# Performance work log

Hardware: AMD Instinct MI355X
Metric: run time of the kernel (lower is better)

The kernel has to match this reference:

```python
import jax, jax.numpy as jnp
import numpy as np

B, S, D, H = 2, 2048, 2048, 16
DK = D // H  # 128


def _rope(x, cos, sin):
    # x: [B,S,H,DK]; pairs (x0,x1),(x2,x3),... rotated as complex numbers
    xr = x[..., 0::2]  # [B,S,H,DK/2]
    xi = x[..., 1::2]
    yr = xr * cos - xi * sin
    yi = xr * sin + xi * cos
    y = jnp.stack([yr, yi], axis=-1)  # [B,S,H,DK/2,2]
    return y.reshape(x.shape)


def setup_inputs() -> dict:
    key = jax.random.key(0)
    ks = jax.random.split(key, 12)
    sc = 1.0 / np.sqrt(D)
    q = jax.random.normal(ks[0], (B, S, D), jnp.float32)
    k = jax.random.normal(ks[1], (B, S, D), jnp.float32)
    v = jax.random.normal(ks[2], (B, S, D), jnp.float32)
    mask = jnp.tril(jnp.ones((S, S), jnp.int32))[None, None]  # causal [1,1,S,S]
    # standard RoPE angles: pos * theta^(-2i/dk)
    theta = 10000.0 ** (-jnp.arange(0, DK, 2, dtype=jnp.float32) / DK)  # [DK/2]
    freqs_angles = jnp.arange(S, dtype=jnp.float32)[:, None] * theta[None, :]  # [S,DK/2]
    wq = jax.random.normal(ks[3], (D, D), jnp.float32) * sc
    bq = jax.random.normal(ks[4], (D,), jnp.float32) * 0.01
    wk = jax.random.normal(ks[5], (D, D), jnp.float32) * sc
    bk = jax.random.normal(ks[6], (D,), jnp.float32) * 0.01
    wv = jax.random.normal(ks[7], (D, D), jnp.float32) * sc
    bv = jax.random.normal(ks[8], (D,), jnp.float32) * 0.01
    wo = jax.random.normal(ks[9], (D, D), jnp.float32) * sc
    bo = jax.random.normal(ks[10], (D,), jnp.float32) * 0.01
    return dict(q=q, k=k, v=v, mask=mask, freqs_angles=freqs_angles,
                wq=wq, bq=bq, wk=wk, bk=bk, wv=wv, bv=bv, wo=wo, bo=bo)


def reference(q, k, v, mask, freqs_angles, wq, bq, wk, bk, wv, bv, wo, bo):
    query = q @ wq.T + bq
    key_ = k @ wk.T + bk
    value = v @ wv.T + bv
    query = query.reshape(B, S, H, DK)
    key_ = key_.reshape(B, S, H, DK)
    value = value.reshape(B, S, H, DK).transpose(0, 2, 1, 3)  # [B,H,S,DK]
    cos = jnp.cos(freqs_angles)[None, :, None, :]  # [1,S,1,DK/2]
    sin = jnp.sin(freqs_angles)[None, :, None, :]
    query = _rope(query, cos, sin).transpose(0, 2, 1, 3)  # [B,H,S,DK]
    key_ = _rope(key_, cos, sin).transpose(0, 2, 1, 3)
    scores = jnp.einsum('bhqd,bhkd->bhqk', query, key_) / jnp.sqrt(jnp.float32(DK))
    scores = jnp.where(mask == 0, jnp.float32(-1e9), scores)
    attn = jax.nn.softmax(scores, axis=-1)  # dropout p=0.0 -> identity
    x = jnp.einsum('bhqk,bhkd->bhqd', attn, value)
    x = x.transpose(0, 2, 1, 3).reshape(B, S, D)
    return x @ wo.T + bo
```

## Files before the change

kernel.cpp:

```cpp
#include <hip/hip_runtime.h>
#include <hip/hip_bf16.h>

#define BB 2
#define SS 2048
#define DD 2048
#define HH 16
#define DKK 128
#define MM (BB*SS)

typedef unsigned short u16;
typedef short bf16x8 __attribute__((ext_vector_type(8)));
typedef unsigned short u16x8 __attribute__((ext_vector_type(8)));
typedef float f32x4 __attribute__((ext_vector_type(4)));

static __device__ __forceinline__ f32x4 mfma_bf16(bf16x8 a, bf16x8 b, f32x4 c) {
  return __builtin_amdgcn_mfma_f32_16x16x32_bf16(a, b, c, 0, 0, 0);
}

static __device__ __forceinline__ u16 f2b(float f) {
  unsigned int u = __float_as_uint(f);
  u = (u + 0x7FFFu + ((u >> 16) & 1u)) >> 16;
  return (u16)u;
}

static __device__ __forceinline__ u16 f2bq(float f) {
  unsigned int r;
  asm("v_cvt_pk_bf16_f32 %0, %1, %2" : "=v"(r) : "v"(f), "v"(f));
  return (u16)r;
}

static __device__ __forceinline__ void gl16(const u16* g, u16* l) {
  __builtin_amdgcn_global_load_lds(
      (const __attribute__((address_space(1))) unsigned int*)(const void*)g,
      (__attribute__((address_space(3))) unsigned int*)(void*)l, 16, 0, 0);
}

struct F2BArgs { const float* src[7]; u16* dst[7]; const float* fa; float* cs; };
__global__ __launch_bounds__(256) void k_f2bf_all(F2BArgs a) {
  int bid = blockIdx.x;
  if (bid >= 20480) {
    const int t0 = ((bid - 20480) * 256 + threadIdx.x) * 8;
    float4 a0 = *reinterpret_cast<const float4*>(a.fa + t0);
    float4 a1 = *reinterpret_cast<const float4*>(a.fa + t0 + 4);
    float4 o0, o1, o2, o3;
    o0.x = cosf(a0.x); o0.y = sinf(a0.x); o0.z = cosf(a0.y); o0.w = sinf(a0.y);
    o1.x = cosf(a0.z); o1.y = sinf(a0.z); o1.z = cosf(a0.w); o1.w = sinf(a0.w);
    o2.x = cosf(a1.x); o2.y = sinf(a1.x); o2.z = cosf(a1.y); o2.w = sinf(a1.y);
    o3.x = cosf(a1.z); o3.y = sinf(a1.z); o3.z = cosf(a1.w); o3.w = sinf(a1.w);
    float* out = a.cs + 2 * t0;
    *reinterpret_cast<float4*>(out)      = o0;
    *reinterpret_cast<float4*>(out + 4)  = o1;
    *reinterpret_cast<float4*>(out + 8)  = o2;
    *reinterpret_cast<float4*>(out + 12) = o3;
    return;
  }
  int buf, local;
  if (bid < 12288) { buf = bid >> 12; local = bid & 4095; }
  else { int t = bid - 12288; buf = 3 + (t >> 11); local = t & 2047; }
  const int i = (local * 256 + threadIdx.x) * 8;
  const float* in = a.src[buf];
  float4 v0 = *reinterpret_cast<const float4*>(in + i);
  float4 v1 = *reinterpret_cast<const float4*>(in + i + 4);
  u16x8 o;
  o[0]=f2b(v0.x); o[1]=f2b(v0.y); o[2]=f2b(v0.z); o[3]=f2b(v0.w);
  o[4]=f2b(v1.x); o[5]=f2b(v1.y); o[6]=f2b(v1.z); o[7]=f2b(v1.w);
  *reinterpret_cast<u16x8*>(a.dst[buf] + i) = o;
}

struct GemmJob { const u16* A; const u16* W; const float* bias; void* out; int mode; };
struct GemmArgs { GemmJob job[3]; };

__global__ __launch_bounds__(256, 2) void k_gemm3(GemmArgs ga, const float* __restrict__ cs) {
  const GemmJob J = ga.job[blockIdx.z];
  const u16* __restrict__ A = J.A;
  const u16* __restrict__ W = J.W;
  const int mode = J.mode;
  const int K = DD, N = DD;
  const int KT = K / 64;

  __shared__ __align__(16) u16 sA[2][128 * 64];
  __shared__ __align__(16) u16 sB[2][128 * 64];
  const int tid = threadIdx.x;
  const int l  = tid & 63;
  const int w  = tid >> 6;
  const int wr = w >> 1, wc = w & 1;
  const int bm = blockIdx.x * 128, bn = blockIdx.y * 128;
  const int lr = l & 15;
  const int lg = l >> 4;

  f32x4 acc[4][4];
#pragma unroll
  for (int mi = 0; mi < 4; mi++)
#pragma unroll
    for (int ni = 0; ni < 4; ni++)
#pragma unroll
      for (int j = 0; j < 4; j++) acc[mi][ni][j] = 0.0f;

  const int srcx = ((l & 7) * 8) ^ ((l >> 3) * 8);
  const u16* gAl = A + (size_t)(bm + w*32 + (l >> 3)) * K + srcx;
  const u16* gBl = W + (size_t)(bn + w*32 + (l >> 3)) * K + srcx;

  const int rx = (lr & 7) * 8;

  auto stage = [&](int kt) {
    u16* dA = &sA[kt & 1][(w * 32) * 64];
    u16* dB = &sB[kt & 1][(w * 32) * 64];
    const int k0 = kt * 64;
#pragma unroll
    for (int i = 0; i < 4; i++) gl16(gAl + (size_t)i*8*K + k0, dA + i * 512);
#pragma unroll
    for (int i = 0; i < 4; i++) gl16(gBl + (size_t)i*8*K + k0, dB + i * 512);
  };

  stage(0);
  __syncthreads();

#pragma unroll 1
  for (int t = 0; t < KT; t++) {
    if (t + 1 < KT) stage(t + 1);
    const u16* a_ = sA[t & 1];
    const u16* b_ = sB[t & 1];
#pragma unroll
    for (int kk = 0; kk < 2; kk++) {
      bf16x8 af[4], bfv[4];
#pragma unroll
      for (int i = 0; i < 4; i++)
        af[i]  = *reinterpret_cast<const bf16x8*>(
            a_ + (wr*64 + i*16 + lr) * 64 + ((kk*32 + lg*8) ^ rx));
#pragma unroll
      for (int i = 0; i < 4; i++)
        bfv[i] = *reinterpret_cast<const bf16x8*>(
            b_ + (wc*64 + i*16 + lr) * 64 + ((kk*32 + lg*8) ^ rx));
#pragma unroll
      for (int mi = 0; mi < 4; mi++)
#pragma unroll
        for (int ni = 0; ni < 4; ni++)
          acc[mi][ni] = mfma_bf16(af[mi], bfv[ni], acc[mi][ni]);
    }
    __syncthreads();
  }

#pragma unroll
  for (int mi = 0; mi < 4; mi++) {
#pragma unroll
    for (int ni = 0; ni < 4; ni++) {
      const int col = bn + wc*64 + ni*16 + lr;
      const float bv = J.bias[col];
#pragma unroll
      for (int r = 0; r < 4; r++) {
        const int row = bm + wr*64 + mi*16 + lg*4 + r;
        float v = acc[mi][ni][r] + bv;
        if (mode & 1) {
          const int s  = row & (SS - 1);
          const int dk = col & (DKK - 1);
          const int p  = dk >> 1;
          const float2 csv = *reinterpret_cast<const float2*>(cs + (size_t)(s*64 + p)*2);
          const float other = __shfl_xor(v, 1);
          const float sgn = (dk & 1) ? csv.y : -csv.y;
          v = v * csv.x + other * sgn;
          if (mode == 3) v *= 0.12751744f;
        }
        if (mode == 2) {
          reinterpret_cast<float*>(J.out)[(size_t)row * N + col] = v;
        } else {
          reinterpret_cast<u16*>(J.out)[(size_t)row * N + col] = f2b(v);
        }
      }
    }
  }
}

__global__ __launch_bounds__(256, 2) void k_attn(const u16* __restrict__ Qp,
                                                 const u16* __restrict__ Kp,
                                                 const u16* __restrict__ Vp,
                                                 u16* __restrict__ Op) {
  const int bid = blockIdx.x;
  int bh, qt;
  if (bid < 256) { bh = bid & 31; qt = 15 - (bid >> 5); }
  else { int b2 = bid - 256; bh = b2 & 31; qt = b2 >> 5; }
  const int h  = bh & 15;
  const int b  = bh >> 4;
  const int tid = threadIdx.x;
  const int l  = tid & 63, w = tid >> 6;
  const int lr = l & 15, lg = l >> 4;

  __shared__ __align__(16) u16 Klds[2 * 64 * 128];
  __shared__ __align__(16) u16 VT[128 * 64];
  __shared__ __align__(16) u16 PL[4][32][72];

  int koff[4];
#pragma unroll
  for (int i = 0; i < 4; i++) {
    const int row = w*16 + i*4 + (l >> 4);
    koff[i] = row * DD + (((l & 15) * 8) ^ ((row & 7) * 8));
  }
  const u16* kbase = Kp + (size_t)b * SS * DD + h * DKK;

  const int k0v = (tid >> 5) * 8;
  const int d0  = (tid & 31) * 4;
  const u16* vbase = Vp + (size_t)b * SS * DD + h * DKK + (size_t)k0v * DD + d0;

  uint2 vr[8];

  auto stageK = [&](int nk, int bufq) {
    const u16* kb = kbase + (size_t)nk * (64 * DD);
    u16* dst = Klds + bufq * 8192 + (w * 16) * 128;
#pragma unroll
    for (int i = 0; i < 4; i++) gl16(kb + koff[i], dst + i * 512);
  };
  auto prefV = [&](int nk) {
    const u16* vb = vbase + (size_t)nk * (64 * DD);
#pragma unroll
    for (int c = 0; c < 8; c++) vr[c] = *reinterpret_cast<const uint2*>(vb + c * DD);
  };

  int cur = 0;
  stageK(0, 0);
  prefV(0);

  bf16x8 qf[2][4];
#pragma unroll
  for (int mt = 0; mt < 2; mt++) {
    const size_t qrow = (size_t)(b*SS + qt*128 + w*32 + mt*16 + lr) * DD + h*DKK;
#pragma unroll
    for (int kk = 0; kk < 4; kk++)
      qf[mt][kk] = *reinterpret_cast<const bf16x8*>(Qp + qrow + kk*32 + lg*8);
  }

  float m[2][4], lsum[2][4];
  f32x4 oacc[2][8];
#pragma unroll
  for (int mt = 0; mt < 2; mt++)
#pragma unroll
    for (int r = 0; r < 4; r++) { m[mt][r] = -INFINITY; lsum[mt][r] = 0.0f; }
#pragma unroll
  for (int mt = 0; mt < 2; mt++)
#pragma unroll
    for (int dt = 0; dt < 8; dt++)
#pragma unroll
      for (int jj = 0; jj < 4; jj++) oacc[mt][dt][jj] = 0.0f;

  const int kvmax = 2 * qt + 1;
#pragma unroll 1
  for (int kv = 0; kv <= kvmax; kv++) {
    __syncthreads();
#pragma unroll
    for (int dj = 0; dj < 4; dj++) {
      const int row = d0 + dj;
      const int col = k0v ^ (((row ^ (row >> 3)) & 7) * 8);
      u16x8 pk;
#pragma unroll
      for (int j = 0; j < 8; j++) pk[j] = reinterpret_cast<const u16*>(&vr[j])[dj];
      *reinterpret_cast<u16x8*>(VT + row * 64 + col) = pk;
    }
    __syncthreads();

    const bool hasnext = (kv < kvmax);
    if (hasnext) {
      prefV(kv + 1);
      stageK(kv + 1, cur ^ 1);
    }

    f32x4 sa[2][4];
#pragma unroll
    for (int mt = 0; mt < 2; mt++)
#pragma unroll
      for (int kt = 0; kt < 4; kt++)
#pragma unroll
        for (int jj = 0; jj < 4; jj++) sa[mt][kt][jj] = 0.0f;
    const u16* kl = Klds + cur * 8192;
    __builtin_amdgcn_s_setprio(1);
#pragma unroll
    for (int kk = 0; kk < 4; kk++) {
#pragma unroll
      for (int kt = 0; kt < 4; kt++) {
        const int row = kt*16 + lr;
        const bf16x8 kf = *reinterpret_cast<const bf16x8*>(
            kl + row * 128 + ((kk*32 + lg*8) ^ ((row & 7) * 8)));
#pragma unroll
        for (int mt = 0; mt < 2; mt++)
          sa[mt][kt] = mfma_bf16(qf[mt][kk], kf, sa[mt][kt]);
      }
    }
    __builtin_amdgcn_s_setprio(0);

    if (kv >= 2 * qt) {
#pragma unroll
      for (int kt = 0; kt < 4; kt++) {
        const int key = kv*64 + kt*16 + lr;
#pragma unroll
        for (int mt = 0; mt < 2; mt++)
#pragma unroll
          for (int r = 0; r < 4; r++) {
            const int qv = qt*128 + w*32 + mt*16 + lg*4 + r;
            if (key > qv) sa[mt][kt][r] = -1e9f;
          }
      }
    }

    float pm[2][4];
#pragma unroll
    for (int mt = 0; mt < 2; mt++)
#pragma unroll
      for (int r = 0; r < 4; r++)
        pm[mt][r] = fmaxf(fmaxf(sa[mt][0][r], sa[mt][1][r]),
                          fmaxf(sa[mt][2][r], sa[mt][3][r]));
    bool ok = true;
#pragma unroll
    for (int mt = 0; mt < 2; mt++)
#pragma unroll
      for (int r = 0; r < 4; r++) ok = ok && (pm[mt][r] <= m[mt][r] + 8.0f);
    if (!__all(ok)) {
#pragma unroll
      for (int mt = 0; mt < 2; mt++)
#pragma unroll
        for (int r = 0; r < 4; r++) {
          float t = pm[mt][r];
#pragma unroll
          for (int d = 1; d < 16; d <<= 1) t = fmaxf(t, __shfl_xor(t, d));
          const float mnew = fmaxf(m[mt][r], t);
          const float corr = exp2f(m[mt][r] - mnew);
          lsum[mt][r] *= corr;
#pragma unroll
          for (int dt = 0; dt < 8; dt++) oacc[mt][dt][r] *= corr;
          m[mt][r] = mnew;
        }
    }

#pragma unroll
    for (int mt = 0; mt < 2; mt++)
#pragma unroll
      for (int r = 0; r < 4; r++) {
        float rs = 0.0f;
#pragma unroll
        for (int kt = 0; kt < 4; kt++) {
          const float e = exp2f(sa[mt][kt][r] - m[mt][r]);
          rs += e;
          PL[w][mt*16 + lg*4 + r][kt*16 + lr] = f2bq(e);
        }
        lsum[mt][r] += rs;
      }

    __builtin_amdgcn_s_setprio(1);
#pragma unroll
    for (int kk2 = 0; kk2 < 2; kk2++) {
      bf16x8 pa[2];
#pragma unroll
      for (int mt = 0; mt < 2; mt++)
        pa[mt] = *reinterpret_cast<const bf16x8*>(&PL[w][mt*16 + lr][kk2*32 + lg*8]);
#pragma unroll
      for (int dt = 0; dt < 8; dt++) {
        const int row = dt*16 + lr;
        const bf16x8 vb = *reinterpret_cast<const bf16x8*>(
            VT + row * 64 + ((kk2*32 + lg*8) ^ (((row ^ (row >> 3)) & 7) * 8)));
#pragma unroll
        for (int mt = 0; mt < 2; mt++)
          oacc[mt][dt] = mfma_bf16(pa[mt], vb, oacc[mt][dt]);
      }
    }
    __builtin_amdgcn_s_setprio(0);

    if (hasnext) cur ^= 1;
  }

  float inv[2][4];
#pragma unroll
  for (int mt = 0; mt < 2; mt++)
#pragma unroll
    for (int r = 0; r < 4; r++) {
      float t = lsum[mt][r];
#pragma unroll
      for (int d = 1; d < 16; d <<= 1) t += __shfl_xor(t, d);
      inv[mt][r] = 1.0f / t;
    }
#pragma unroll
  for (int mt = 0; mt < 2; mt++)
#pragma unroll
    for (int dt = 0; dt < 8; dt++)
#pragma unroll
      for (int r = 0; r < 4; r++) {
        const size_t row = (size_t)(b*SS + qt*128 + w*32 + mt*16 + lg*4 + r);
        Op[row * DD + h*DKK + dt*16 + lr] = f2bq(oacc[mt][dt][r] * inv[mt][r]);
      }
}

extern "C" void kernel_launch(void* const* d_in, const int* in_sizes, int n_in,
                              void* d_out, int out_size, void* d_ws, size_t ws_size,
                              hipStream_t stream) {
  const float* q  = (const float*)d_in[0];
  const float* k  = (const float*)d_in[1];
  const float* v  = (const float*)d_in[2];
  const float* fa = (const float*)d_in[4];
  const float* wq = (const float*)d_in[5];
  const float* bq = (const float*)d_in[6];
  const float* wk = (const float*)d_in[7];
  const float* bk = (const float*)d_in[8];
  const float* wv = (const float*)d_in[9];
  const float* bv = (const float*)d_in[10];
  const float* wo = (const float*)d_in[11];
  const float* bo = (const float*)d_in[12];

  float* cs = (float*)d_ws;
  u16* bf = (u16*)((char*)d_ws + (size_t)262144 * sizeof(float));
  const size_t NX = (size_t)MM * DD;
  const size_t NW = (size_t)DD * DD;
  u16* q_bf  = bf;
  u16* k_bf  = q_bf + NX;
  u16* v_bf  = k_bf + NX;
  u16* wq_bf = v_bf + NX;
  u16* wk_bf = wq_bf + NW;
  u16* wv_bf = wk_bf + NW;
  u16* wo_bf = wv_bf + NW;
  u16* Qp    = wo_bf + NW;
  u16* Kp    = Qp + NX;
  u16* Vp    = Kp + NX;
  u16* Ao    = Vp + NX;

  F2BArgs fa7;
  fa7.src[0] = q;  fa7.dst[0] = q_bf;
  fa7.src[1] = k;  fa7.dst[1] = k_bf;
  fa7.src[2] = v;  fa7.dst[2] = v_bf;
  fa7.src[3] = wq; fa7.dst[3] = wq_bf;
  fa7.src[4] = wk; fa7.dst[4] = wk_bf;
  fa7.src[5] = wv; fa7.dst[5] = wv_bf;
  fa7.src[6] = wo; fa7.dst[6] = wo_bf;
  fa7.fa = fa;     fa7.cs = cs;
  k_f2bf_all<<<dim3(20544), 256, 0, stream>>>(fa7);

  GemmArgs gq;
  gq.job[0] = GemmJob{ q_bf, wq_bf, bq, (void*)Qp, 3 };
  gq.job[1] = GemmJob{ k_bf, wk_bf, bk, (void*)Kp, 1 };
  gq.job[2] = GemmJob{ v_bf, wv_bf, bv, (void*)Vp, 0 };
  k_gemm3<<<dim3(MM/128, DD/128, 3), 256, 0, stream>>>(gq, cs);

  k_attn<<<dim3(512), 256, 0, stream>>>(Qp, Kp, Vp, Ao);

  GemmArgs go;
  go.job[0] = GemmJob{ Ao, wo_bf, bo, d_out, 2 };
  go.job[1] = go.job[0];
  go.job[2] = go.job[0];
  k_gemm3<<<dim3(MM/128, DD/128, 1), 256, 0, stream>>>(go, cs);
}
```

Baseline: 310.8 us.

## Fuse fp32-to-bf16 activation conversion into QKV GEMM A-tile loading

The QKV projection GEMM now reads fp32 q/k/v directly, converting to bf16 in registers with packed cvt and writing swizzled tiles into LDS after the MFMA loop. The prep kernel converts only weights and computes cos/sin, avoiding a full write-and-reread of the bf16 activation copies. The cost is doubled A-operand global traffic per tile, with repeated reads across N tiles, plus extra register use and loss of direct-to-LDS loads for A.

New measurement: 375.9 us. 21.0% more time.

```diff
diff --git a/kernel.cpp b/kernel.cpp
--- a/kernel.cpp
+++ b/kernel.cpp
@@ -23,11 +23,12 @@
   return (u16)u;
 }
 
-static __device__ __forceinline__ u16 f2bq(float f) {
+static __device__ __forceinline__ unsigned int cvt2(float lo, float hi) {
   unsigned int r;
-  asm("v_cvt_pk_bf16_f32 %0, %1, %2" : "=v"(r) : "v"(f), "v"(f));
-  return (u16)r;
-}
+  asm("v_cvt_pk_bf16_f32 %0, %1, %2" : "=v"(r) : "v"(lo), "v"(hi));
+  return r;
+}
+static __device__ __forceinline__ u16 f2bq(float f) { return (u16)cvt2(f, f); }
 
 static __device__ __forceinline__ void gl16(const u16* g, u16* l) {
   __builtin_amdgcn_global_load_lds(
@@ -35,11 +36,11 @@
       (__attribute__((address_space(3))) unsigned int*)(void*)l, 16, 0, 0);
 }
 
-struct F2BArgs { const float* src[7]; u16* dst[7]; const float* fa; float* cs; };
-__global__ __launch_bounds__(256) void k_f2bf_all(F2BArgs a) {
+struct F2BArgs { const float* src[4]; u16* dst[4]; const float* fa; float* cs; };
+__global__ __launch_bounds__(256) void k_f2bf_w(F2BArgs a) {
   int bid = blockIdx.x;
-  if (bid >= 20480) {
-    const int t0 = ((bid - 20480) * 256 + threadIdx.x) * 8;
+  if (bid >= 8192) {
+    const int t0 = ((bid - 8192) * 256 + threadIdx.x) * 8;
     float4 a0 = *reinterpret_cast<const float4*>(a.fa + t0);
     float4 a1 = *reinterpret_cast<const float4*>(a.fa + t0 + 4);
     float4 o0, o1, o2, o3;
@@ -54,9 +55,8 @@
     *reinterpret_cast<float4*>(out + 12) = o3;
     return;
   }
-  int buf, local;
-  if (bid < 12288) { buf = bid >> 12; local = bid & 4095; }
-  else { int t = bid - 12288; buf = 3 + (t >> 11); local = t & 2047; }
+  const int buf = bid >> 11;
+  const int local = bid & 2047;
   const int i = (local * 256 + threadIdx.x) * 8;
   const float* in = a.src[buf];
   float4 v0 = *reinterpret_cast<const float4*>(in + i);
@@ -67,12 +67,12 @@
   *reinterpret_cast<u16x8*>(a.dst[buf] + i) = o;
 }
 
-struct GemmJob { const u16* A; const u16* W; const float* bias; void* out; int mode; };
+struct GemmJob { const void* A; const u16* W; const float* bias; void* out; int mode; };
 struct GemmArgs { GemmJob job[3]; };
 
-__global__ __launch_bounds__(256, 2) void k_gemm3(GemmArgs ga, const float* __restrict__ cs) {
+template <int AF32>
+__global__ __launch_bounds__(256, 2) void k_gemmT(GemmArgs ga, const float* __restrict__ cs) {
   const GemmJob J = ga.job[blockIdx.z];
-  const u16* __restrict__ A = J.A;
   const u16* __restrict__ W = J.W;
   const int mode = J.mode;
   const int K = DD, N = DD;
@@ -97,27 +97,61 @@
       for (int j = 0; j < 4; j++) acc[mi][ni][j] = 0.0f;
 
   const int srcx = ((l & 7) * 8) ^ ((l >> 3) * 8);
-  const u16* gAl = A + (size_t)(bm + w*32 + (l >> 3)) * K + srcx;
+  const int cx   = srcx;
+  const u16* gAl16 = (const u16*)J.A + (size_t)(bm + w*32 + (l >> 3)) * K + srcx;
+  const float* gA32 = (const float*)J.A + (size_t)(bm + w*32 + (l >> 3)) * K + (l & 7) * 8;
   const u16* gBl = W + (size_t)(bn + w*32 + (l >> 3)) * K + srcx;
+  const int rowbase = (w*32 + (l >> 3)) * 64;
 
   const int rx = (lr & 7) * 8;
 
-  auto stage = [&](int kt) {
+  float4 ar[4][2];
+
+  auto loadA32 = [&](int kt) {
+    const float* g = gA32 + kt * 64;
+#pragma unroll
+    for (int i = 0; i < 4; i++) {
+      ar[i][0] = *reinterpret_cast<const float4*>(g + (size_t)i*8*K);
+      ar[i][1] = *reinterpret_cast<const float4*>(g + (size_t)i*8*K + 4);
+    }
+  };
+  auto writeA32 = [&](int kt) {
+    u16* dA = &sA[kt & 1][0];
+#pragma unroll
+    for (int i = 0; i < 4; i++) {
+      uint4 o;
+      o.x = cvt2(ar[i][0].x, ar[i][0].y);
+      o.y = cvt2(ar[i][0].z, ar[i][0].w);
+      o.z = cvt2(ar[i][1].x, ar[i][1].y);
+      o.w = cvt2(ar[i][1].z, ar[i][1].w);
+      *reinterpret_cast<uint4*>(dA + rowbase + i*8*64 + cx) = o;
+    }
+  };
+  auto stageA16 = [&](int kt) {
     u16* dA = &sA[kt & 1][(w * 32) * 64];
+    const int k0 = kt * 64;
+#pragma unroll
+    for (int i = 0; i < 4; i++) gl16(gAl16 + (size_t)i*8*K + k0, dA + i * 512);
+  };
+  auto stageB = [&](int kt) {
     u16* dB = &sB[kt & 1][(w * 32) * 64];
     const int k0 = kt * 64;
 #pragma unroll
-    for (int i = 0; i < 4; i++) gl16(gAl + (size_t)i*8*K + k0, dA + i * 512);
-#pragma unroll
     for (int i = 0; i < 4; i++) gl16(gBl + (size_t)i*8*K + k0, dB + i * 512);
   };
 
-  stage(0);
+  stageB(0);
+  if (AF32) { loadA32(0); writeA32(0); }
+  else      { stageA16(0); }
   __syncthreads();
 
 #pragma unroll 1
   for (int t = 0; t < KT; t++) {
-    if (t + 1 < KT) stage(t + 1);
+    if (t + 1 < KT) {
+      stageB(t + 1);
+      if (AF32) loadA32(t + 1);
+      else      stageA16(t + 1);
+    }
     const u16* a_ = sA[t & 1];
     const u16* b_ = sB[t & 1];
 #pragma unroll
@@ -137,6 +171,7 @@
         for (int ni = 0; ni < 4; ni++)
           acc[mi][ni] = mfma_bf16(af[mi], bfv[ni], acc[mi][ni]);
     }
+    if (AF32 && t + 1 < KT) writeA32(t + 1);
     __syncthreads();
   }
 
@@ -416,28 +451,25 @@
   u16* Vp    = Kp + NX;
   u16* Ao    = Vp + NX;
 
-  F2BArgs fa7;
-  fa7.src[0] = q;  fa7.dst[0] = q_bf;
-  fa7.src[1] = k;  fa7.dst[1] = k_bf;
-  fa7.src[2] = v;  fa7.dst[2] = v_bf;
-  fa7.src[3] = wq; fa7.dst[3] = wq_bf;
-  fa7.src[4] = wk; fa7.dst[4] = wk_bf;
-  fa7.src[5] = wv; fa7.dst[5] = wv_bf;
-  fa7.src[6] = wo; fa7.dst[6] = wo_bf;
-  fa7.fa = fa;     fa7.cs = cs;
-  k_f2bf_all<<<dim3(20544), 256, 0, stream>>>(fa7);
+  F2BArgs fw;
+  fw.src[0] = wq; fw.dst[0] = wq_bf;
+  fw.src[1] = wk; fw.dst[1] = wk_bf;
+  fw.src[2] = wv; fw.dst[2] = wv_bf;
+  fw.src[3] = wo; fw.dst[3] = wo_bf;
+  fw.fa = fa;     fw.cs = cs;
+  k_f2bf_w<<<dim3(8256), 256, 0, stream>>>(fw);
 
   GemmArgs gq;
-  gq.job[0] = GemmJob{ q_bf, wq_bf, bq, (void*)Qp, 3 };
-  gq.job[1] = GemmJob{ k_bf, wk_bf, bk, (void*)Kp, 1 };
-  gq.job[2] = GemmJob{ v_bf, wv_bf, bv, (void*)Vp, 0 };
-  k_gemm3<<<dim3(MM/128, DD/128, 3), 256, 0, stream>>>(gq, cs);
+  gq.job[0] = GemmJob{ (const void*)q, wq_bf, bq, (void*)Qp, 3 };
+  gq.job[1] = GemmJob{ (const void*)k, wk_bf, bk, (void*)Kp, 1 };
+  gq.job[2] = GemmJob{ (const void*)v, wv_bf, bv, (void*)Vp, 0 };
+  k_gemmT<1><<<dim3(MM/128, DD/128, 3), 256, 0, stream>>>(gq, cs);
 
   k_attn<<<dim3(512), 256, 0, stream>>>(Qp, Kp, Vp, Ao);
 
   GemmArgs go;
-  go.job[0] = GemmJob{ Ao, wo_bf, bo, d_out, 2 };
+  go.job[0] = GemmJob{ (const void*)Ao, wo_bf, bo, d_out, 2 };
   go.job[1] = go.job[0];
   go.job[2] = go.job[0];
-  k_gemm3<<<dim3(MM/128, DD/128, 1), 256, 0, stream>>>(go, cs);
-}
+  k_gemmT<0><<<dim3(MM/128, DD/128, 1), 256, 0, stream>>>(go, cs);
+}
```

## Halve attention query tile to 64 rows and double grid size

Applied to the files above, without the earlier changes.

The attention kernel now processes 64 query rows per block (16 per wave) instead of 128, launching 1024 blocks in longest-first order. This cuts per-block registers and causal waste on the diagonal tile, and gives more blocks to balance across CUs. In exchange, each K/V tile loaded into LDS is reused by half as many queries, so K/V global traffic and staging overhead per FLOP roughly double.

Result: faster. 304.3 us (-2.1%).

```diff
diff --git a/kernel.cpp b/kernel.cpp
--- a/kernel.cpp
+++ b/kernel.cpp
@@ -175,18 +175,18 @@
                                                  const u16* __restrict__ Vp,
                                                  u16* __restrict__ Op) {
   const int bid = blockIdx.x;
-  int bh, qt;
-  if (bid < 256) { bh = bid & 31; qt = 15 - (bid >> 5); }
-  else { int b2 = bid - 256; bh = b2 & 31; qt = b2 >> 5; }
+  const int j  = 31 - (bid >> 5);
+  const int bh = bid & 31;
   const int h  = bh & 15;
   const int b  = bh >> 4;
   const int tid = threadIdx.x;
   const int l  = tid & 63, w = tid >> 6;
   const int lr = l & 15, lg = l >> 4;
+  const int q0 = j * 64;
 
   __shared__ __align__(16) u16 Klds[2 * 64 * 128];
   __shared__ __align__(16) u16 VT[128 * 64];
-  __shared__ __align__(16) u16 PL[4][32][72];
+  __shared__ __align__(16) u16 PL[4][16][72];
 
   int koff[4];
 #pragma unroll
@@ -218,31 +218,25 @@
   stageK(0, 0);
   prefV(0);
 
-  bf16x8 qf[2][4];
-#pragma unroll
-  for (int mt = 0; mt < 2; mt++) {
-    const size_t qrow = (size_t)(b*SS + qt*128 + w*32 + mt*16 + lr) * DD + h*DKK;
+  bf16x8 qf[4];
+  {
+    const size_t qrow = (size_t)(b*SS + q0 + w*16 + lr) * DD + h*DKK;
 #pragma unroll
     for (int kk = 0; kk < 4; kk++)
-      qf[mt][kk] = *reinterpret_cast<const bf16x8*>(Qp + qrow + kk*32 + lg*8);
-  }
-
-  float m[2][4], lsum[2][4];
-  f32x4 oacc[2][8];
-#pragma unroll
-  for (int mt = 0; mt < 2; mt++)
-#pragma unroll
-    for (int r = 0; r < 4; r++) { m[mt][r] = -INFINITY; lsum[mt][r] = 0.0f; }
-#pragma unroll
-  for (int mt = 0; mt < 2; mt++)
-#pragma unroll
-    for (int dt = 0; dt < 8; dt++)
-#pragma unroll
-      for (int jj = 0; jj < 4; jj++) oacc[mt][dt][jj] = 0.0f;
-
-  const int kvmax = 2 * qt + 1;
+      qf[kk] = *reinterpret_cast<const bf16x8*>(Qp + qrow + kk*32 + lg*8);
+  }
+
+  float m[4], lsum[4];
+  f32x4 oacc[8];
+#pragma unroll
+  for (int r = 0; r < 4; r++) { m[r] = -INFINITY; lsum[r] = 0.0f; }
+#pragma unroll
+  for (int dt = 0; dt < 8; dt++)
+#pragma unroll
+    for (int jj = 0; jj < 4; jj++) oacc[dt][jj] = 0.0f;
+
 #pragma unroll 1
-  for (int kv = 0; kv <= kvmax; kv++) {
+  for (int kv = 0; kv <= j; kv++) {
     __syncthreads();
 #pragma unroll
     for (int dj = 0; dj < 4; dj++) {
@@ -250,24 +244,22 @@
       const int col = k0v ^ (((row ^ (row >> 3)) & 7) * 8);
       u16x8 pk;
 #pragma unroll
-      for (int j = 0; j < 8; j++) pk[j] = reinterpret_cast<const u16*>(&vr[j])[dj];
+      for (int jq = 0; jq < 8; jq++) pk[jq] = reinterpret_cast<const u16*>(&vr[jq])[dj];
       *reinterpret_cast<u16x8*>(VT + row * 64 + col) = pk;
     }
     __syncthreads();
 
-    const bool hasnext = (kv < kvmax);
+    const bool hasnext = (kv < j);
     if (hasnext) {
       prefV(kv + 1);
       stageK(kv + 1, cur ^ 1);
     }
 
-    f32x4 sa[2][4];
-#pragma unroll
-    for (int mt = 0; mt < 2; mt++)
-#pragma unroll
-      for (int kt = 0; kt < 4; kt++)
-#pragma unroll
-        for (int jj = 0; jj < 4; jj++) sa[mt][kt][jj] = 0.0f;
+    f32x4 sa[4];
+#pragma unroll
+    for (int kt = 0; kt < 4; kt++)
+#pragma unroll
+      for (int jj = 0; jj < 4; jj++) sa[kt][jj] = 0.0f;
     const u16* kl = Klds + cur * 8192;
     __builtin_amdgcn_s_setprio(1);
 #pragma unroll
@@ -277,85 +269,67 @@
         const int row = kt*16 + lr;
         const bf16x8 kf = *reinterpret_cast<const bf16x8*>(
             kl + row * 128 + ((kk*32 + lg*8) ^ ((row & 7) * 8)));
-#pragma unroll
-        for (int mt = 0; mt < 2; mt++)
-          sa[mt][kt] = mfma_bf16(qf[mt][kk], kf, sa[mt][kt]);
+        sa[kt] = mfma_bf16(qf[kk], kf, sa[kt]);
       }
     }
     __builtin_amdgcn_s_setprio(0);
 
-    if (kv >= 2 * qt) {
+    if (kv == j) {
 #pragma unroll
       for (int kt = 0; kt < 4; kt++) {
-        const int key = kv*64 + kt*16 + lr;
-#pragma unroll
-        for (int mt = 0; mt < 2; mt++)
-#pragma unroll
-          for (int r = 0; r < 4; r++) {
-            const int qv = qt*128 + w*32 + mt*16 + lg*4 + r;
-            if (key > qv) sa[mt][kt][r] = -1e9f;
-          }
-      }
-    }
-
-    float pm[2][4];
-#pragma unroll
-    for (int mt = 0; mt < 2; mt++)
-#pragma unroll
-      for (int r = 0; r < 4; r++)
-        pm[mt][r] = fmaxf(fmaxf(sa[mt][0][r], sa[mt][1][r]),
-                          fmaxf(sa[mt][2][r], sa[mt][3][r]));
+        const int key = kt*16 + lr;
+#pragma unroll
+        for (int r = 0; r < 4; r++) {
+          const int qv = w*16 + lg*4 + r;
+          if (key > qv) sa[kt][r] = -1e9f;
+        }
+      }
+    }
+
+    float pm[4];
+#pragma unroll
+    for (int r = 0; r < 4; r++)
+      pm[r] = fmaxf(fmaxf(sa[0][r], sa[1][r]), fmaxf(sa[2][r], sa[3][r]));
     bool ok = true;
 #pragma unroll
-    for (int mt = 0; mt < 2; mt++)
-#pragma unroll
-      for (int r = 0; r < 4; r++) ok = ok && (pm[mt][r] <= m[mt][r] + 8.0f);
+    for (int r = 0; r < 4; r++) ok = ok && (pm[r] <= m[r] + 8.0f);
     if (!__all(ok)) {
 #pragma unroll
-      for (int mt = 0; mt < 2; mt++)
-#pragma unroll
-        for (int r = 0; r < 4; r++) {
-          float t = pm[mt][r];
-#pragma unroll
-          for (int d = 1; d < 16; d <<= 1) t = fmaxf(t, __shfl_xor(t, d));
-          const float mnew = fmaxf(m[mt][r], t);
-          const float corr = exp2f(m[mt][r] - mnew);
-          lsum[mt][r] *= corr;
-#pragma unroll
-          for (int dt = 0; dt < 8; dt++) oacc[mt][dt][r] *= corr;
-          m[mt][r] = mnew;
-        }
-    }
-
-#pragma unroll
-    for (int mt = 0; mt < 2; mt++)
-#pragma unroll
       for (int r = 0; r < 4; r++) {
-        float rs = 0.0f;
-#pragma unroll
-        for (int kt = 0; kt < 4; kt++) {
-          const float e = exp2f(sa[mt][kt][r] - m[mt][r]);
-          rs += e;
-          PL[w][mt*16 + lg*4 + r][kt*16 + lr] = f2bq(e);
-        }
-        lsum[mt][r] += rs;
-      }
+        float t = pm[r];
+#pragma unroll
+        for (int d = 1; d < 16; d <<= 1) t = fmaxf(t, __shfl_xor(t, d));
+        const float mnew = fmaxf(m[r], t);
+        const float corr = exp2f(m[r] - mnew);
+        lsum[r] *= corr;
+#pragma unroll
+        for (int dt = 0; dt < 8; dt++) oacc[dt][r] *= corr;
+        m[r] = mnew;
+      }
+    }
+
+#pragma unroll
+    for (int r = 0; r < 4; r++) {
+      float rs = 0.0f;
+#pragma unroll
+      for (int kt = 0; kt < 4; kt++) {
+        const float e = exp2f(sa[kt][r] - m[r]);
+        rs += e;
+        PL[w][lg*4 + r][kt*16 + lr] = f2bq(e);
+      }
+      lsum[r] += rs;
+    }
 
     __builtin_amdgcn_s_setprio(1);
 #pragma unroll
     for (int kk2 = 0; kk2 < 2; kk2++) {
-      bf16x8 pa[2];
-#pragma unroll
-      for (int mt = 0; mt < 2; mt++)
-        pa[mt] = *reinterpret_cast<const bf16x8*>(&PL[w][mt*16 + lr][kk2*32 + lg*8]);
+      const bf16x8 pa = *reinterpret_cast<const bf16x8*>(&PL[w][lr][kk2*32 + lg*8]);
 #pragma unroll
       for (int dt = 0; dt < 8; dt++) {
         const int row = dt*16 + lr;
         const bf16x8 vb = *reinterpret_cast<const bf16x8*>(
             VT + row * 64 + ((kk2*32 + lg*8) ^ (((row ^ (row >> 3)) & 7) * 8)));
-#pragma unroll
-        for (int mt = 0; mt < 2; mt++)
-          oacc[mt][dt] = mfma_bf16(pa[mt], vb, oacc[mt][dt]);
+        oacc[dt] = mfma_bf16(pa, vb, oacc[dt]);
       }
     }
     __builtin_amdgcn_s_setprio(0);
@@ -363,25 +337,21 @@
     if (hasnext) cur ^= 1;
   }
 
-  float inv[2][4];
-#pragma unroll
-  for (int mt = 0; mt < 2; mt++)
+  float inv[4];
+#pragma unroll
+  for (int r = 0; r < 4; r++) {
+    float t = lsum[r];
+#pragma unroll
+    for (int d = 1; d < 16; d <<= 1) t += __shfl_xor(t, d);
+    inv[r] = 1.0f / t;
+  }
+#pragma unroll
+  for (int dt = 0; dt < 8; dt++)
 #pragma unroll
     for (int r = 0; r < 4; r++) {
-      float t = lsum[mt][r];
-#pragma unroll
-      for (int d = 1; d < 16; d <<= 1) t += __shfl_xor(t, d);
-      inv[mt][r] = 1.0f / t;
-    }
-#pragma unroll
-  for (int mt = 0; mt < 2; mt++)
-#pragma unroll
-    for (int dt = 0; dt < 8; dt++)
-#pragma unroll
-      for (int r = 0; r < 4; r++) {
-        const size_t row = (size_t)(b*SS + qt*128 + w*32 + mt*16 + lg*4 + r);
-        Op[row * DD + h*DKK + dt*16 + lr] = f2bq(oacc[mt][dt][r] * inv[mt][r]);
-      }
+      const size_t row = (size_t)(b*SS + q0 + w*16 + lg*4 + r);
+      Op[row * DD + h*DKK + dt*16 + lr] = f2bq(oacc[dt][r] * inv[r]);
+    }
 }
 
 extern "C" void kernel_launch(void* const* d_in, const int* in_sizes, int n_in,
@@ -433,7 +403,7 @@
   gq.job[2] = GemmJob{ v_bf, wv_bf, bv, (void*)Vp, 0 };
   k_gemm3<<<dim3(MM/128, DD/128, 3), 256, 0, stream>>>(gq, cs);
 
-  k_attn<<<dim3(512), 256, 0, stream>>>(Qp, Kp, Vp, Ao);
+  k_attn<<<dim3(1024), 256, 0, stream>>>(Qp, Kp, Vp, Ao);
 
   GemmArgs go;
   go.job[0] = GemmJob{ Ao, wo_bf, bo, d_out, 2 };
```

## Split KV range across two wave groups and pair causal query tiles per block

Applied to the files above, without the earlier changes.

The attention kernel now runs 512 threads per block. Two 4-wave groups each process alternating 64-key tiles for the same 128-row query tile, and their partial softmax states (max, sum, accumulator) are merged through LDS at the end. Each block also handles a complementary pair of query tiles (15-p and p), which evens out causal work and halves the grid to 256 blocks. This aims for better load balance and more latency hiding per CU, at the cost of extra LDS (double K/V buffers), a merge step with extra barriers, and possibly lower occupancy.

After: 311.9 us. Within noise of the previous version (+0.4%).

```diff
diff --git a/kernel.cpp b/kernel.cpp
--- a/kernel.cpp
+++ b/kernel.cpp
@@ -170,218 +170,255 @@
   }
 }
 
-__global__ __launch_bounds__(256, 2) void k_attn(const u16* __restrict__ Qp,
+__global__ __launch_bounds__(512, 2) void k_attn(const u16* __restrict__ Qp,
                                                  const u16* __restrict__ Kp,
                                                  const u16* __restrict__ Vp,
                                                  u16* __restrict__ Op) {
   const int bid = blockIdx.x;
-  int bh, qt;
-  if (bid < 256) { bh = bid & 31; qt = 15 - (bid >> 5); }
-  else { int b2 = bid - 256; bh = b2 & 31; qt = b2 >> 5; }
+  const int p  = bid >> 5;
+  const int bh = bid & 31;
   const int h  = bh & 15;
   const int b  = bh >> 4;
   const int tid = threadIdx.x;
-  const int l  = tid & 63, w = tid >> 6;
+  const int l  = tid & 63;
+  const int w  = tid >> 6;
+  const int g  = w >> 2;
+  const int wg = w & 3;
   const int lr = l & 15, lg = l >> 4;
 
-  __shared__ __align__(16) u16 Klds[2 * 64 * 128];
-  __shared__ __align__(16) u16 VT[128 * 64];
-  __shared__ __align__(16) u16 PL[4][32][72];
+  __shared__ __align__(16) u16 Klds[2][2][64 * 128];
+  __shared__ __align__(16) u16 VT[2][128 * 64];
+  __shared__ __align__(16) u16 PL[2][4][32][72];
+  __shared__ float mlbuf[128][2];
 
   int koff[4];
 #pragma unroll
   for (int i = 0; i < 4; i++) {
-    const int row = w*16 + i*4 + (l >> 4);
+    const int row = wg*16 + i*4 + (l >> 4);
     koff[i] = row * DD + (((l & 15) * 8) ^ ((row & 7) * 8));
   }
   const u16* kbase = Kp + (size_t)b * SS * DD + h * DKK;
 
-  const int k0v = (tid >> 5) * 8;
-  const int d0  = (tid & 31) * 4;
+  const int gtid = tid & 255;
+  const int k0v = (gtid >> 5) * 8;
+  const int d0  = (gtid & 31) * 4;
   const u16* vbase = Vp + (size_t)b * SS * DD + h * DKK + (size_t)k0v * DD + d0;
 
   uint2 vr[8];
 
-  auto stageK = [&](int nk, int bufq) {
-    const u16* kb = kbase + (size_t)nk * (64 * DD);
-    u16* dst = Klds + bufq * 8192 + (w * 16) * 128;
+  auto stageK = [&](int s, int bufq) {
+    const u16* kb = kbase + (size_t)s * (64 * DD);
+    u16* dst = &Klds[g][bufq][(wg * 16) * 128];
 #pragma unroll
     for (int i = 0; i < 4; i++) gl16(kb + koff[i], dst + i * 512);
   };
-  auto prefV = [&](int nk) {
-    const u16* vb = vbase + (size_t)nk * (64 * DD);
+  auto prefV = [&](int s) {
+    const u16* vb = vbase + (size_t)s * (64 * DD);
 #pragma unroll
     for (int c = 0; c < 8; c++) vr[c] = *reinterpret_cast<const uint2*>(vb + c * DD);
   };
 
-  int cur = 0;
-  stageK(0, 0);
-  prefV(0);
-
-  bf16x8 qf[2][4];
-#pragma unroll
-  for (int mt = 0; mt < 2; mt++) {
-    const size_t qrow = (size_t)(b*SS + qt*128 + w*32 + mt*16 + lr) * DD + h*DKK;
-#pragma unroll
-    for (int kk = 0; kk < 4; kk++)
-      qf[mt][kk] = *reinterpret_cast<const bf16x8*>(Qp + qrow + kk*32 + lg*8);
+#pragma unroll 1
+  for (int half = 0; half < 2; half++) {
+    const int jj = half ? p : (15 - p);
+    const int q0 = jj * 128;
+
+    bf16x8 qf[2][4];
+#pragma unroll
+    for (int mt = 0; mt < 2; mt++) {
+      const size_t qrow = (size_t)(b*SS + q0 + wg*32 + mt*16 + lr) * DD + h*DKK;
+#pragma unroll
+      for (int kk = 0; kk < 4; kk++)
+        qf[mt][kk] = *reinterpret_cast<const bf16x8*>(Qp + qrow + kk*32 + lg*8);
+    }
+
+    float m[2][4], lsum[2][4];
+    f32x4 oacc[2][8];
+#pragma unroll
+    for (int mt = 0; mt < 2; mt++)
+#pragma unroll
+      for (int r = 0; r < 4; r++) { m[mt][r] = -30000.0f; lsum[mt][r] = 0.0f; }
+#pragma unroll
+    for (int mt = 0; mt < 2; mt++)
+#pragma unroll
+      for (int dt = 0; dt < 8; dt++)
+#pragma unroll
+        for (int jq = 0; jq < 4; jq++) oacc[mt][dt][jq] = 0.0f;
+
+    int cur = 0;
+    stageK(g, 0);
+    prefV(g);
+
+#pragma unroll 1
+    for (int u = 0; u <= jj; u++) {
+      __syncthreads();
+#pragma unroll
+      for (int dj = 0; dj < 4; dj++) {
+        const int row = d0 + dj;
+        const int col = k0v ^ (((row ^ (row >> 3)) & 7) * 8);
+        u16x8 pk;
+#pragma unroll
+        for (int jq = 0; jq < 8; jq++) pk[jq] = reinterpret_cast<const u16*>(&vr[jq])[dj];
+        *reinterpret_cast<u16x8*>(&VT[g][row * 64 + col]) = pk;
+      }
+      __syncthreads();
+
+      const bool hasnext = (u < jj);
+      if (hasnext) {
+        prefV(2*(u+1) + g);
+        stageK(2*(u+1) + g, cur ^ 1);
+      }
+
+      f32x4 sa[2][4];
+#pragma unroll
+      for (int mt = 0; mt < 2; mt++)
+#pragma unroll
+        for (int kt = 0; kt < 4; kt++)
+#pragma unroll
+          for (int jq = 0; jq < 4; jq++) sa[mt][kt][jq] = 0.0f;
+      const u16* kl = &Klds[g][cur][0];
+      __builtin_amdgcn_s_setprio(1);
+#pragma unroll
+      for (int kk = 0; kk < 4; kk++) {
+#pragma unroll
+        for (int kt = 0; kt < 4; kt++) {
+          const int row = kt*16 + lr;
+          const bf16x8 kf = *reinterpret_cast<const bf16x8*>(
+              kl + row * 128 + ((kk*32 + lg*8) ^ ((row & 7) * 8)));
+#pragma unroll
+          for (int mt = 0; mt < 2; mt++)
+            sa[mt][kt] = mfma_bf16(qf[mt][kk], kf, sa[mt][kt]);
+        }
+      }
+      __builtin_amdgcn_s_setprio(0);
+
+      if (u == jj) {
+#pragma unroll
+        for (int kt = 0; kt < 4; kt++) {
+          const int key = g*64 + kt*16 + lr;
+#pragma unroll
+          for (int mt = 0; mt < 2; mt++)
+#pragma unroll
+            for (int r = 0; r < 4; r++) {
+              const int lrow = wg*32 + mt*16 + lg*4 + r;
+              if (key > lrow) sa[mt][kt][r] = -1e9f;
+            }
+        }
+      }
+
+      float pm[2][4];
+#pragma unroll
+      for (int mt = 0; mt < 2; mt++)
+#pragma unroll
+        for (int r = 0; r < 4; r++)
+          pm[mt][r] = fmaxf(fmaxf(sa[mt][0][r], sa[mt][1][r]),
+                            fmaxf(sa[mt][2][r], sa[mt][3][r]));
+      bool ok = true;
+#pragma unroll
+      for (int mt = 0; mt < 2; mt++)
+#pragma unroll
+        for (int r = 0; r < 4; r++) ok = ok && (pm[mt][r] <= m[mt][r] + 8.0f);
+      if (!__all(ok)) {
+#pragma unroll
+        for (int mt = 0; mt < 2; mt++)
+#pragma unroll
+          for (int r = 0; r < 4; r++) {
+            float t = pm[mt][r];
+#pragma unroll
+            for (int d = 1; d < 16; d <<= 1) t = fmaxf(t, __shfl_xor(t, d));
+            const float mnew = fmaxf(m[mt][r], t);
+            const float corr = exp2f(m[mt][r] - mnew);
+            lsum[mt][r] *= corr;
+#pragma unroll
+            for (int dt = 0; dt < 8; dt++) oacc[mt][dt][r] *= corr;
+            m[mt][r] = mnew;
+          }
+      }
+
+#pragma unroll
+      for (int mt = 0; mt < 2; mt++)
+#pragma unroll
+        for (int r = 0; r < 4; r++) {
+          float rs = 0.0f;
+#pragma unroll
+          for (int kt = 0; kt < 4; kt++) {
+            const float e = exp2f(sa[mt][kt][r] - m[mt][r]);
+            rs += e;
+            PL[g][wg][mt*16 + lg*4 + r][kt*16 + lr] = f2bq(e);
+          }
+          lsum[mt][r] += rs;
+        }
+
+      __builtin_amdgcn_s_setprio(1);
+#pragma unroll
+      for (int kk2 = 0; kk2 < 2; kk2++) {
+        bf16x8 pa[2];
+#pragma unroll
+        for (int mt = 0; mt < 2; mt++)
+          pa[mt] = *reinterpret_cast<const bf16x8*>(&PL[g][wg][mt*16 + lr][kk2*32 + lg*8]);
+#pragma unroll
+        for (int dt = 0; dt < 8; dt++) {
+          const int row = dt*16 + lr;
+          const bf16x8 vb = *reinterpret_cast<const bf16x8*>(
+              &VT[g][row * 64 + ((kk2*32 + lg*8) ^ (((row ^ (row >> 3)) & 7) * 8))]);
+#pragma unroll
+          for (int mt = 0; mt < 2; mt++)
+            oacc[mt][dt] = mfma_bf16(pa[mt], vb, oacc[mt][dt]);
+        }
+      }
+      __builtin_amdgcn_s_setprio(0);
+
+      if (hasnext) cur ^= 1;
+    }
+
+    float lred[2][4];
+#pragma unroll
+    for (int mt = 0; mt < 2; mt++)
+#pragma unroll
+      for (int r = 0; r < 4; r++) {
+        float t = lsum[mt][r];
+#pragma unroll
+        for (int d = 1; d < 16; d <<= 1) t += __shfl_xor(t, d);
+        lred[mt][r] = t;
+      }
+
+    __syncthreads();
+    float* ob = (float*)&Klds[0][0][0];
+    if (g == 1) {
+#pragma unroll
+      for (int mt = 0; mt < 2; mt++)
+#pragma unroll
+        for (int r = 0; r < 4; r++) {
+          const int lrow = wg*32 + mt*16 + lg*4 + r;
+          if (lr == 0) { mlbuf[lrow][0] = m[mt][r]; mlbuf[lrow][1] = lred[mt][r]; }
+#pragma unroll
+          for (int dt = 0; dt < 8; dt++)
+            ob[lrow * 128 + dt*16 + lr] = oacc[mt][dt][r];
+        }
+    }
+    __syncthreads();
+    if (g == 0) {
+#pragma unroll
+      for (int mt = 0; mt < 2; mt++)
+#pragma unroll
+        for (int r = 0; r < 4; r++) {
+          const int lrow = wg*32 + mt*16 + lg*4 + r;
+          const float m1 = mlbuf[lrow][0];
+          const float l1 = mlbuf[lrow][1];
+          const float ms = fmaxf(m[mt][r], m1);
+          const float c0 = exp2f(m[mt][r] - ms);
+          const float c1 = exp2f(m1 - ms);
+          const float inv = 1.0f / (lred[mt][r] * c0 + l1 * c1);
+          const size_t row = (size_t)(b*SS + q0 + lrow);
+#pragma unroll
+          for (int dt = 0; dt < 8; dt++) {
+            const float o = (oacc[mt][dt][r] * c0 + ob[lrow * 128 + dt*16 + lr] * c1) * inv;
+            Op[row * DD + h*DKK + dt*16 + lr] = f2bq(o);
+          }
+        }
+    }
+    __syncthreads();
   }
-
-  float m[2][4], lsum[2][4];
-  f32x4 oacc[2][8];
-#pragma unroll
-  for (int mt = 0; mt < 2; mt++)
-#pragma unroll
-    for (int r = 0; r < 4; r++) { m[mt][r] = -INFINITY; lsum[mt][r] = 0.0f; }
-#pragma unroll
-  for (int mt = 0; mt < 2; mt++)
-#pragma unroll
-    for (int dt = 0; dt < 8; dt++)
-#pragma unroll
-      for (int jj = 0; jj < 4; jj++) oacc[mt][dt][jj] = 0.0f;
-
-  const int kvmax = 2 * qt + 1;
-#pragma unroll 1
-  for (int kv = 0; kv <= kvmax; kv++) {
-    __syncthreads();
-#pragma unroll
-    for (int dj = 0; dj < 4; dj++) {
-      const int row = d0 + dj;
-      const int col = k0v ^ (((row ^ (row >> 3)) & 7) * 8);
-      u16x8 pk;
-#pragma unroll
-      for (int j = 0; j < 8; j++) pk[j] = reinterpret_cast<const u16*>(&vr[j])[dj];
-      *reinterpret_cast<u16x8*>(VT + row * 64 + col) = pk;
-    }
-    __syncthreads();
-
-    const bool hasnext = (kv < kvmax);
-    if (hasnext) {
-      prefV(kv + 1);
-      stageK(kv + 1, cur ^ 1);
-    }
-
-    f32x4 sa[2][4];
-#pragma unroll
-    for (int mt = 0; mt < 2; mt++)
-#pragma unroll
-      for (int kt = 0; kt < 4; kt++)
-#pragma unroll
-        for (int jj = 0; jj < 4; jj++) sa[mt][kt][jj] = 0.0f;
-    const u16* kl = Klds + cur * 8192;
-    __builtin_amdgcn_s_setprio(1);
-#pragma unroll
-    for (int kk = 0; kk < 4; kk++) {
-#pragma unroll
-      for (int kt = 0; kt < 4; kt++) {
-        const int row = kt*16 + lr;
-        const bf16x8 kf = *reinterpret_cast<const bf16x8*>(
-            kl + row * 128 + ((kk*32 + lg*8) ^ ((row & 7) * 8)));
-#pragma unroll
-        for (int mt = 0; mt < 2; mt++)
-          sa[mt][kt] = mfma_bf16(qf[mt][kk], kf, sa[mt][kt]);
-      }
-    }
-    __builtin_amdgcn_s_setprio(0);
-
-    if (kv >= 2 * qt) {
-#pragma unroll
-      for (int kt = 0; kt < 4; kt++) {
-        const int key = kv*64 + kt*16 + lr;
-#pragma unroll
-        for (int mt = 0; mt < 2; mt++)
-#pragma unroll
-          for (int r = 0; r < 4; r++) {
-            const int qv = qt*128 + w*32 + mt*16 + lg*4 + r;
-            if (key > qv) sa[mt][kt][r] = -1e9f;
-          }
-      }
-    }
-
-    float pm[2][4];
-#pragma unroll
-    for (int mt = 0; mt < 2; mt++)
-#pragma unroll
-      for (int r = 0; r < 4; r++)
-        pm[mt][r] = fmaxf(fmaxf(sa[mt][0][r], sa[mt][1][r]),
-                          fmaxf(sa[mt][2][r], sa[mt][3][r]));
-    bool ok = true;
-#pragma unroll
-    for (int mt = 0; mt < 2; mt++)
-#pragma unroll
-      for (int r = 0; r < 4; r++) ok = ok && (pm[mt][r] <= m[mt][r] + 8.0f);
-    if (!__all(ok)) {
-#pragma unroll
-      for (int mt = 0; mt < 2; mt++)
-#pragma unroll
-        for (int r = 0; r < 4; r++) {
-          float t = pm[mt][r];
-#pragma unroll
-          for (int d = 1; d < 16; d <<= 1) t = fmaxf(t, __shfl_xor(t, d));
-          const float mnew = fmaxf(m[mt][r], t);
-          const float corr = exp2f(m[mt][r] - mnew);
-          lsum[mt][r] *= corr;
-#pragma unroll
-          for (int dt = 0; dt < 8; dt++) oacc[mt][dt][r] *= corr;
-          m[mt][r] = mnew;
-        }
-    }
-
-#pragma unroll
-    for (int mt = 0; mt < 2; mt++)
-#pragma unroll
-      for (int r = 0; r < 4; r++) {
-        float rs = 0.0f;
-#pragma unroll
-        for (int kt = 0; kt < 4; kt++) {
-          const float e = exp2f(sa[mt][kt][r] - m[mt][r]);
-          rs += e;
-          PL[w][mt*16 + lg*4 + r][kt*16 + lr] = f2bq(e);
-        }
-        lsum[mt][r] += rs;
-      }
-
-    __builtin_amdgcn_s_setprio(1);
-#pragma unroll
-    for (int kk2 = 0; kk2 < 2; kk2++) {
-      bf16x8 pa[2];
-#pragma unroll
-      for (int mt = 0; mt < 2; mt++)
-        pa[mt] = *reinterpret_cast<const bf16x8*>(&PL[w][mt*16 + lr][kk2*32 + lg*8]);
-#pragma unroll
-      for (int dt = 0; dt < 8; dt++) {
-        const int row = dt*16 + lr;
-        const bf16x8 vb = *reinterpret_cast<const bf16x8*>(
-            VT + row * 64 + ((kk2*32 + lg*8) ^ (((row ^ (row >> 3)) & 7) * 8)));
-#pragma unroll
-        for (int mt = 0; mt < 2; mt++)
-          oacc[mt][dt] = mfma_bf16(pa[mt], vb, oacc[mt][dt]);
-      }
-    }
-    __builtin_amdgcn_s_setprio(0);
-
-    if (hasnext) cur ^= 1;
-  }
-
-  float inv[2][4];
-#pragma unroll
-  for (int mt = 0; mt < 2; mt++)
-#pragma unroll
-    for (int r = 0; r < 4; r++) {
-      float t = lsum[mt][r];
-#pragma unroll
-      for (int d = 1; d < 16; d <<= 1) t += __shfl_xor(t, d);
-      inv[mt][r] = 1.0f / t;
-    }
-#pragma unroll
-  for (int mt = 0; mt < 2; mt++)
-#pragma unroll
-    for (int dt = 0; dt < 8; dt++)
-#pragma unroll
-      for (int r = 0; r < 4; r++) {
-        const size_t row = (size_t)(b*SS + qt*128 + w*32 + mt*16 + lg*4 + r);
-        Op[row * DD + h*DKK + dt*16 + lr] = f2bq(oacc[mt][dt][r] * inv[mt][r]);
-      }
 }
 
 extern "C" void kernel_launch(void* const* d_in, const int* in_sizes, int n_in,
@@ -433,7 +470,7 @@
   gq.job[2] = GemmJob{ v_bf, wv_bf, bv, (void*)Vp, 0 };
   k_gemm3<<<dim3(MM/128, DD/128, 3), 256, 0, stream>>>(gq, cs);
 
-  k_attn<<<dim3(512), 256, 0, stream>>>(Qp, Kp, Vp, Ao);
+  k_attn<<<dim3(256), 512, 0, stream>>>(Qp, Kp, Vp, Ao);
 
   GemmArgs go;
   go.job[0] = GemmJob{ Ao, wo_bf, bo, d_out, 2 };
```
